# Optimization experiments

Hardware: AMD Instinct MI355X
Metric: run time of the kernel (lower is better)

Reference implementation:

```python
import jax, jax.numpy as jnp
import numpy as np

D_MODEL = 1024
SEL_DIM = 64
CONFIGS = [(4, 32), (8, 64), (16, 128)]  # (heads, dim)
B, T = 2, 2048


def setup_inputs() -> dict:
    key = jax.random.key(0)
    ks = jax.random.split(key, 20)
    s = 0.02  # init scale for stability
    inp = {
        "x": jax.random.normal(ks[0], (B, T, D_MODEL), jnp.float32),
        "sel_w1": jax.random.normal(ks[1], (SEL_DIM, D_MODEL), jnp.float32) * s,
        "sel_b1": jnp.zeros((SEL_DIM,), jnp.float32),
        "sel_w2": jax.random.normal(ks[2], (SEL_DIM, SEL_DIM), jnp.float32) * s,
        "sel_b2": jnp.zeros((SEL_DIM,), jnp.float32),
        "sel_w3": jax.random.normal(ks[3], (len(CONFIGS), SEL_DIM), jnp.float32) * s,
        "sel_b3": jnp.zeros((len(CONFIGS),), jnp.float32),
    }
    for i, (h, d) in enumerate(CONFIGS):
        inp[f"qw{i}"] = jax.random.normal(ks[4 + 3 * i], (h * d, D_MODEL), jnp.float32) * s
        inp[f"kw{i}"] = jax.random.normal(ks[5 + 3 * i], (d, D_MODEL), jnp.float32) * s
        inp[f"ww{i}"] = jax.random.normal(ks[6 + 3 * i], (h, D_MODEL), jnp.float32) * s
    return inp


def _seq_features(x):
    # x: [b,t,d]
    b, t, d = x.shape
    seq_mean = jnp.mean(x, axis=1, keepdims=True)            # [b,1,d]
    seq_std = jnp.std(x, axis=1, keepdims=True, ddof=1)      # torch.std is unbiased
    pos = (jnp.arange(t, dtype=x.dtype) / t)[None, :, None]  # [1,t,1] broadcast to [b,t,d]
    return x + seq_mean + seq_std + pos * 0.1


def _forward(x, sel_w1, sel_b1, sel_w2, sel_b2, sel_w3, sel_b3,
             qw0, kw0, ww0, qw1, kw1, ww1, qw2, kw2, ww2):
    b, t, dm = x.shape
    feats = _seq_features(x)
    h1 = jax.nn.relu(feats @ sel_w1.T + sel_b1)
    h2 = jax.nn.relu(h1 @ sel_w2.T + sel_b2)
    config_probs = jax.nn.softmax(h2 @ sel_w3.T + sel_b3, axis=-1)  # [b,t,ncfg]

    per_cfg = [(qw0, kw0, ww0), (qw1, kw1, ww1), (qw2, kw2, ww2)]
    final = jnp.zeros((b, t, t), dtype=x.dtype)
    for i, ((heads, dim), (qw, kw, ww)) in enumerate(zip(CONFIGS, per_cfg)):
        q = (x @ qw.T).reshape(b, t, heads, dim)   # [b,t,h,d]
        k = x @ kw.T                               # [b,s,d]
        w = x @ ww.T                               # [b,t,h]
        dots = jnp.einsum('bthd,bsd->bths', q, k)  # [b,t,h,s]
        score = jnp.einsum('bths,bth->bts', jax.nn.relu(dots), w)  # relu*weight, sum heads
        final = final + config_probs[:, :, i:i + 1] * score
    return final


def reference(x, sel_w1, sel_b1, sel_w2, sel_b2, sel_w3, sel_b3,
              qw0, kw0, ww0, qw1, kw1, ww1, qw2, kw2, ww2):
    return _forward(x, sel_w1, sel_b1, sel_w2, sel_b2, sel_w3, sel_b3,
                    qw0, kw0, ww0, qw1, kw1, ww1, qw2, kw2, ww2)
```

## Files before the change

### kernel.cpp

```cpp
#include <hip/hip_runtime.h>
#include <hip/hip_fp16.h>
#include <cstdint>
#include <cstddef>
#include <math.h>

#define B_ 2
#define T_ 2048
#define D_ 1024
#define M_ (B_*T_)

#define QO0 0
#define KO0 128
#define WO0 160
#define QO1 168
#define KO1 680
#define WO1 744
#define QO2 752
#define KO2 2800
#define WO2 2928
#define SELO 2944
#define LDN 3072

typedef float f32x16 __attribute__((ext_vector_type(16)));
typedef short bf16x8 __attribute__((ext_vector_type(8)));
typedef unsigned short u16;

__device__ __forceinline__ u16 f2bf(float f) {
    unsigned int u = __float_as_uint(f);
    unsigned int r = (u + 0x7fffu + ((u >> 16) & 1u)) >> 16;
    return (u16)r;
}
__device__ __forceinline__ float bf2f(u16 b) {
    return __uint_as_float(((unsigned int)b) << 16);
}

__device__ __forceinline__ void gload16(const void* g, void* l) {
    __builtin_amdgcn_global_load_lds(
        (const __attribute__((address_space(1))) unsigned int*)g,
        (__attribute__((address_space(3))) unsigned int*)l,
        16, 0, 0);
}

__device__ __forceinline__ void stage_plane(const u16* src_base, int row_stride, int k0,
                                            int rg, int lane, u16* dst) {
    int rl  = lane >> 2;
    int row = rg * 16 + rl;
    int q   = (lane & 3) ^ (rl & 3) ^ ((rl >> 2) & 3);
    const u16* s = src_base + (size_t)row * row_stride + k0 + q * 8;
    gload16(s, dst + rg * 512);
}

__global__ void stats1(const float* __restrict__ x, float* __restrict__ part,
                       float* __restrict__ part2, u16* __restrict__ Xh) {
    int d4 = threadIdx.x * 4;
    int tc = blockIdx.x;
    int b  = blockIdx.y;
    size_t base = (size_t)b * T_ * D_ + (size_t)tc * 16 * D_ + d4;
    float4 s = make_float4(0.f, 0.f, 0.f, 0.f);
    float4 s2 = make_float4(0.f, 0.f, 0.f, 0.f);
#pragma unroll
    for (int t = 0; t < 16; ++t) {
        float4 v = *(const float4*)(x + base + (size_t)t * D_);
        s.x += v.x; s.y += v.y; s.z += v.z; s.w += v.w;
        s2.x += v.x * v.x; s2.y += v.y * v.y; s2.z += v.z * v.z; s2.w += v.w * v.w;
        ushort4 h;
        h.x = f2bf(v.x); h.y = f2bf(v.y); h.z = f2bf(v.z); h.w = f2bf(v.w);
        *(ushort4*)(Xh + base + (size_t)t * D_) = h;
    }
    *(float4*)(part  + (size_t)(b * 128 + tc) * D_ + d4) = s;
    *(float4*)(part2 + (size_t)(b * 128 + tc) * D_ + d4) = s2;
}

__global__ void stats2(const float* __restrict__ part, const float* __restrict__ part2,
                       const float* __restrict__ w1,
                       float* __restrict__ msd, float* __restrict__ s1) {
    __shared__ float msL[1024];
    __shared__ float ps[64][17];
    __shared__ float pw[64][17];
    int b = blockIdx.x, tid = threadIdx.x;
    float s = 0.f, s2 = 0.f;
#pragma unroll 8
    for (int i = 0; i < 128; ++i) {
        s  += part [(b * 128 + i) * D_ + tid];
        s2 += part2[(b * 128 + i) * D_ + tid];
    }
    float mean = s / (float)T_;
    float var  = (s2 - (float)T_ * mean * mean) / (float)(T_ - 1);
    msL[tid] = mean + sqrtf(fmaxf(var, 0.f));
    __syncthreads();
    int j = tid >> 4, cc = tid & 15;
    float am = 0.f, aw = 0.f;
    const float* wr = w1 + (size_t)j * D_ + cc * 64;
    const float* mr = msL + cc * 64;
    for (int dd = 0; dd < 64; ++dd) { float w = wr[dd]; am += mr[dd] * w; aw += w; }
    ps[j][cc] = am; pw[j][cc] = aw;
    __syncthreads();
    if (tid < 64) {
        float sm = 0.f, sw = 0.f;
        for (int i = 0; i < 16; ++i) { sm += ps[tid][i]; sw += pw[tid][i]; }
        msd[b * 64 + tid] = sm;
        if (b == 0) s1[tid] = sw;
    }
}

__global__ void split_w(const float* __restrict__ qw0, const float* __restrict__ kw0,
                        const float* __restrict__ ww0, const float* __restrict__ qw1,
                        const float* __restrict__ kw1, const float* __restrict__ ww1,
                        const float* __restrict__ qw2, const float* __restrict__ kw2,
                        const float* __restrict__ ww2, const float* __restrict__ w1s,
                        u16* __restrict__ Wh) {
    int row = blockIdx.x;
    int col = threadIdx.x * 4;
    const float* src = nullptr;
    if      (row < 128)  src = qw0 + (size_t)row * D_;
    else if (row < 160)  src = kw0 + (size_t)(row - 128) * D_;
    else if (row < 164)  src = ww0 + (size_t)(row - 160) * D_;
    else if (row < 168)  src = nullptr;
    else if (row < 680)  src = qw1 + (size_t)(row - 168) * D_;
    else if (row < 744)  src = kw1 + (size_t)(row - 680) * D_;
    else if (row < 752)  src = ww1 + (size_t)(row - 744) * D_;
    else if (row < 2800) src = qw2 + (size_t)(row - 752) * D_;
    else if (row < 2928) src = kw2 + (size_t)(row - 2800) * D_;
    else if (row < 2944) src = ww2 + (size_t)(row - 2928) * D_;
    else if (row < 3008) src = w1s + (size_t)(row - 2944) * D_;
    float4 v = src ? *(const float4*)(src + col) : make_float4(0.f, 0.f, 0.f, 0.f);
    ushort4 h;
    h.x = f2bf(v.x); h.y = f2bf(v.y); h.z = f2bf(v.z); h.w = f2bf(v.w);
    *(ushort4*)&Wh[(size_t)row * D_ + col] = h;
}

__global__ __launch_bounds__(256, 3) void proj_gemm(
    const u16* __restrict__ Xh, const u16* __restrict__ Wh, u16* __restrict__ Ph) {
    __shared__ u16 As[8192], Bs[8192];
    int tid = threadIdx.x;
    int wave = tid >> 6, lane = tid & 63;
    int bm = blockIdx.x * 128, bn = blockIdx.y * 128;
    int wt = wave >> 1, wn = wave & 1;
    int fm = lane & 31, hv = lane >> 5;
    int tkey = (fm & 3) ^ ((fm >> 2) & 3);
    f32x16 acc[2][2];
#pragma unroll
    for (int i = 0; i < 2; ++i)
#pragma unroll
        for (int j = 0; j < 2; ++j)
#pragma unroll
            for (int r = 0; r < 16; ++r) acc[i][j][r] = 0.f;

    const u16* xh = Xh + (size_t)bm * D_;
    const u16* wh = Wh + (size_t)bn * D_;

    for (int kc = 0; kc < 16; ++kc) {
        int k0 = kc * 64;
#pragma unroll
        for (int i = 0; i < 8; ++i) {
            int j = wave * 8 + i;
            int mat = j >> 4;
            int pl  = (j >> 3) & 1;
            int rg  = j & 7;
            stage_plane(mat ? wh : xh, D_, k0 + pl * 32, rg, lane,
                        (mat ? Bs : As) + pl * 4096);
        }
        __syncthreads();
#pragma unroll
        for (int ks = 0; ks < 4; ++ks) {
            int pl = ks >> 1;
            int slot8 = (((ks & 1) * 2 + hv) ^ tkey) * 8;
            bf16x8 a_h[2], b_h[2];
#pragma unroll
            for (int t = 0; t < 2; ++t) {
                a_h[t] = *(const bf16x8*)&As[pl * 4096 + (wt * 64 + t * 32 + fm) * 32 + slot8];
                b_h[t] = *(const bf16x8*)&Bs[pl * 4096 + (wn * 64 + t * 32 + fm) * 32 + slot8];
            }
#pragma unroll
            for (int ti = 0; ti < 2; ++ti)
#pragma unroll
                for (int tj = 0; tj < 2; ++tj)
                    acc[ti][tj] = __builtin_amdgcn_mfma_f32_32x32x16_bf16(a_h[ti], b_h[tj], acc[ti][tj], 0, 0, 0);
        }
        __syncthreads();
    }
#pragma unroll
    for (int ti = 0; ti < 2; ++ti)
#pragma unroll
        for (int tj = 0; tj < 2; ++tj)
#pragma unroll
            for (int r = 0; r < 16; ++r) {
                int row = bm + wt * 64 + ti * 32 + (r & 3) + 8 * (r >> 2) + 4 * hv;
                int col = bn + wn * 64 + tj * 32 + fm;
                Ph[(size_t)row * LDN + col] = f2bf(acc[ti][tj][r]);
            }
}

__global__ void selector2(const u16* __restrict__ Ph,
                          const float* __restrict__ msd, const float* __restrict__ s1,
                          const float* __restrict__ b1, const float* __restrict__ w2,
                          const float* __restrict__ b2, const float* __restrict__ w3,
                          const float* __restrict__ b3, __half* __restrict__ WP) {
    __shared__ float h1s[4][64];
    __shared__ float h2s[4][64];
    __shared__ float lg[4][3];
    int tid = threadIdx.x;
    int slot = tid >> 6, j = tid & 63;
    int bt = blockIdx.x * 4 + slot;
    int b = bt >> 11, t = bt & 2047;
    size_t pidx = (size_t)bt * LDN + SELO + j;
    float v = bf2f(Ph[pidx])
            + msd[b * 64 + j] + 0.1f * ((float)t / (float)T_) * s1[j] + b1[j];
    h1s[slot][j] = fmaxf(v, 0.f);
    __syncthreads();
    float a2 = b2[j];
    {
        const float4* w2v = (const float4*)(w2 + (size_t)j * 64);
        const float4* h1v = (const float4*)h1s[slot];
#pragma unroll
        for (int d = 0; d < 16; ++d) {
            float4 wv = w2v[d], hv4 = h1v[d];
            a2 = fmaf(hv4.x, wv.x, a2);
            a2 = fmaf(hv4.y, wv.y, a2);
            a2 = fmaf(hv4.z, wv.z, a2);
            a2 = fmaf(hv4.w, wv.w, a2);
        }
    }
    h2s[slot][j] = fmaxf(a2, 0.f);
    __syncthreads();
    if (j < 3) {
        float a3 = b3[j];
        const float4* w3v = (const float4*)(w3 + (size_t)j * 64);
        const float4* h2v = (const float4*)h2s[slot];
#pragma unroll
        for (int d = 0; d < 16; ++d) {
            float4 wv = w3v[d], hv4 = h2v[d];
            a3 = fmaf(hv4.x, wv.x, a3);
            a3 = fmaf(hv4.y, wv.y, a3);
            a3 = fmaf(hv4.z, wv.z, a3);
            a3 = fmaf(hv4.w, wv.w, a3);
        }
        lg[slot][j] = a3;
    }
    __syncthreads();
    if (j < 28) {
        float m = fmaxf(lg[slot][0], fmaxf(lg[slot][1], lg[slot][2]));
        float e0 = expf(lg[slot][0] - m), e1 = expf(lg[slot][1] - m), e2 = expf(lg[slot][2] - m);
        float inv = 1.f / (e0 + e1 + e2);
        int wcol = (j < 4) ? (WO0 + j) : ((j < 12) ? (WO1 + j - 4) : (WO2 + j - 12));
        float p = ((j < 4) ? e0 : ((j < 12) ? e1 : e2)) * inv;
        float w = bf2f(Ph[(size_t)bt * LDN + wcol]);
        WP[(size_t)(b * 28 + j) * T_ + t] = __float2half(w * p);
    }
}

__device__ __forceinline__ int qcol_of(int c) {
    if (c < 2)  return QO0 + c * 64;
    if (c < 10) return QO1 + (c - 2) * 64;
    return QO2 + (c - 10) * 64;
}

__global__ __launch_bounds__(256, 2) void score_kernel(
    const u16* __restrict__ Ph, const __half* __restrict__ WP, float* __restrict__ out) {
    __shared__ u16 Qs[2][8192];
    __shared__ u16 Ks[4 * 4096];
    __shared__ __half wpL[3584];
    int tid = threadIdx.x;
    int wave = tid >> 6, lane = tid & 63;
    int wt = wave >> 1, wn = wave & 1;
    int fm = lane & 31, hv = lane >> 5;
    int tkey = (fm & 3) ^ ((fm >> 2) & 3);

    int n = blockIdx.z * 256 + blockIdx.y * 16 + blockIdx.x;
    int p = (n & 7) * 4 + (n >> 7);
    int xb = (n >> 3) & 15;
    int b = p >> 4, yb = p & 15;
    int t0 = yb * 128, s0 = xb * 128;

    const u16* Pq = Ph + (size_t)(b * T_ + t0) * LDN;
    const u16* Pk = Ph + (size_t)(b * T_ + s0) * LDN;

    auto stageQ = [&](int buf, int qcol) {
#pragma unroll
        for (int i = 0; i < 4; ++i) {
            int j = (wave << 2) + i;
            int pl = j >> 3, rg = j & 7;
            stage_plane(Pq, LDN, qcol + pl * 32, rg, lane, &Qs[buf][pl * 4096]);
        }
    };

#pragma unroll
    for (int i = 0; i < 6; ++i) {
        int j = i * 4 + wave;
        int pl = j >> 3, rg = j & 7;
        int col = (pl == 0) ? KO0 : ((pl == 1) ? KO1 : KO1 + 32);
        stage_plane(Pk, LDN, col, rg, lane, &Ks[pl * 4096]);
    }
#pragma unroll
    for (int i = 0; i < 2; ++i) {
        int j = i * 4 + wave;
        if (j < 7) {
            const __half* src = WP + (size_t)(b * 28 + j * 4 + (lane >> 4)) * T_ + t0 + (lane & 15) * 8;
            gload16(src, (u16*)wpL + j * 512);
        }
    }
    stageQ(0, QO0);

    f32x16 outacc[2][2], dots[2][2], Z16;
#pragma unroll
    for (int r = 0; r < 16; ++r) Z16[r] = 0.f;
#pragma unroll
    for (int i = 0; i < 2; ++i)
#pragma unroll
        for (int j = 0; j < 2; ++j)
#pragma unroll
            for (int r = 0; r < 16; ++r) { outacc[i][j][r] = 0.f; dots[i][j][r] = 0.f; }

    auto epi = [&](int g) {
#pragma unroll
        for (int ti = 0; ti < 2; ++ti) {
            int rowbase = wt * 64 + ti * 32 + 4 * hv;
#pragma unroll
            for (int rq = 0; rq < 4; ++rq) {
                __half2 wpq[2];
                *(short4*)wpq = *(const short4*)&wpL[g * 128 + rowbase + rq * 8];
                float2 f01 = __half22float2(wpq[0]);
                float2 f23 = __half22float2(wpq[1]);
                float wv[4] = {f01.x, f01.y, f23.x, f23.y};
#pragma unroll
                for (int tj = 0; tj < 2; ++tj)
#pragma unroll
                    for (int r2 = 0; r2 < 4; ++r2) {
                        int r = rq * 4 + r2;
                        outacc[ti][tj][r] += fmaxf(dots[ti][tj][r], 0.f) * wv[r2];
                    }
            }
        }
    };

    auto runPhase = [&](int c, int kpA, int kpB, bool z0, bool midBreak,
                        int gMid, bool hasEnd, int gEnd) {
        if (c + 1 < 42) {
            stageQ((c + 1) & 1, qcol_of(c + 1));
            asm volatile("s_waitcnt vmcnt(4)" ::: "memory");
        } else {
            asm volatile("s_waitcnt vmcnt(0)" ::: "memory");
        }
        __builtin_amdgcn_s_barrier();
        __builtin_amdgcn_sched_barrier(0);
        const u16* qb = Qs[c & 1];

        bf16x8 kf[2][2], qf[2][2];
        auto loadks = [&](int ks, int sl) {
            int kp = (ks < 2) ? kpA : kpB;
            int slot8 = (((ks & 1) * 2 + hv) ^ tkey) * 8;
#pragma unroll
            for (int tj = 0; tj < 2; ++tj)
                kf[sl][tj] = *(const bf16x8*)&Ks[kp * 4096 + (wn * 64 + tj * 32 + fm) * 32 + slot8];
#pragma unroll
            for (int ti = 0; ti < 2; ++ti)
                qf[sl][ti] = *(const bf16x8*)&qb[(ks >> 1) * 4096 + (wt * 64 + ti * 32 + fm) * 32 + slot8];
        };
        loadks(0, 0);
#pragma unroll
        for (int ks = 0; ks < 4; ++ks) {
            if (ks < 3) loadks(ks + 1, (ks + 1) & 1);
            bool zero = (ks == 0 && z0) || (ks == 2 && midBreak);
            int sl = ks & 1;
            __builtin_amdgcn_s_setprio(1);
#pragma unroll
            for (int ti = 0; ti < 2; ++ti)
#pragma unroll
                for (int tj = 0; tj < 2; ++tj)
                    dots[ti][tj] = __builtin_amdgcn_mfma_f32_32x32x16_bf16(
                        qf[sl][ti], kf[sl][tj], zero ? Z16 : dots[ti][tj], 0, 0, 0);
            __builtin_amdgcn_s_setprio(0);
            if (ks == 1 && midBreak) epi(gMid);
            if (ks == 3 && hasEnd)   epi(gEnd);
        }
        __builtin_amdgcn_sched_barrier(0);
        __builtin_amdgcn_s_barrier();
    };

#pragma unroll
    for (int c = 0; c < 2; ++c)
        runPhase(c, 0, 0, true, true, 2 * c, true, 2 * c + 1);
    for (int h = 0; h < 8; ++h) {
        runPhase(2 + h, 1, 2, true, false, -1, true, 4 + h);
        if (h == 7) {
            for (int j = wave; j < 32; j += 4) {
                int pl = j >> 3, rg = j & 7;
                stage_plane(Pk, LDN, KO2 + pl * 32, rg, lane, &Ks[pl * 4096]);
            }
        }
    }
    for (int h = 0; h < 16; ++h) {
        runPhase(10 + 2 * h, 0, 1, true, false, -1, false, -1);
        runPhase(11 + 2 * h, 2, 3, false, false, -1, true, 12 + h);
    }

#pragma unroll
    for (int ti = 0; ti < 2; ++ti)
#pragma unroll
        for (int tj = 0; tj < 2; ++tj)
#pragma unroll
            for (int r = 0; r < 16; ++r) {
                int trow = wt * 64 + ti * 32 + (r & 3) + 8 * (r >> 2) + 4 * hv;
                int scol = wn * 64 + tj * 32 + fm;
                __builtin_nontemporal_store(outacc[ti][tj][r],
                    &out[(size_t)(b * T_ + t0 + trow) * T_ + (s0 + scol)]);
            }
}

extern "C" void kernel_launch(void* const* d_in, const int* in_sizes, int n_in,
                              void* d_out, int out_size, void* d_ws, size_t ws_size,
                              hipStream_t stream) {
    const float* x   = (const float*)d_in[0];
    const float* w1  = (const float*)d_in[1];
    const float* b1  = (const float*)d_in[2];
    const float* w2  = (const float*)d_in[3];
    const float* b2  = (const float*)d_in[4];
    const float* w3  = (const float*)d_in[5];
    const float* b3  = (const float*)d_in[6];
    const float* qw0 = (const float*)d_in[7];
    const float* kw0 = (const float*)d_in[8];
    const float* ww0 = (const float*)d_in[9];
    const float* qw1 = (const float*)d_in[10];
    const float* kw1 = (const float*)d_in[11];
    const float* ww1 = (const float*)d_in[12];
    const float* qw2 = (const float*)d_in[13];
    const float* kw2 = (const float*)d_in[14];
    const float* ww2 = (const float*)d_in[15];
    float* out = (float*)d_out;

    float* fb = (float*)d_ws;
    float* PA  = fb; fb += (size_t)B_ * 128 * D_;
    float* PA2 = fb; fb += (size_t)B_ * 128 * D_;
    float* MSD = fb; fb += 128;
    float* S1  = fb; fb += 64;
    __half* WP = (__half*)fb; fb += (size_t)B_ * 28 * T_ / 2;
    u16* ub = (u16*)fb;
    u16* Wh = ub; ub += (size_t)LDN * D_;
    u16* Xh = ub; ub += (size_t)M_ * D_;
    u16* Ph = ub; ub += (size_t)M_ * LDN;

    stats1<<<dim3(128, B_), 256, 0, stream>>>(x, PA, PA2, Xh);
    stats2<<<dim3(B_), 1024, 0, stream>>>(PA, PA2, w1, MSD, S1);
    split_w<<<dim3(LDN), 256, 0, stream>>>(qw0, kw0, ww0, qw1, kw1, ww1,
                                           qw2, kw2, ww2, w1, Wh);
    proj_gemm<<<dim3(M_ / 128, LDN / 128), 256, 0, stream>>>(Xh, Wh, Ph);
    selector2<<<dim3(M_ / 4), 256, 0, stream>>>(Ph, MSD, S1, b1, w2, b2, w3, b3, WP);
    score_kernel<<<dim3(T_ / 128, T_ / 128, B_), 256, 0, stream>>>(Ph, WP, out);
}
```

Before: 256.4 us.

## Fuse stats and weight-cast kernels; precompute LDS pointers and fp32 weights in score kernel

Merges stats1 and split_w into a single prep launch, which removes one kernel launch and lets the two independent jobs run concurrently. In score_kernel, the per-head weight tile is converted to fp32 in LDS once up front instead of being converted in the epilogue. Per-lane global and LDS base pointers are now precomputed, so the inner loop does less address arithmetic. The fragment double-buffering (prefetching the next k-step's loads) is dropped in favour of straight loads per k-step. This adds a __syncthreads and doubles the wp LDS footprint, and it risks exposing more LDS latency because the loads are no longer prefetched.

```diff
diff --git a/kernel.cpp b/kernel.cpp
--- a/kernel.cpp
+++ b/kernel.cpp
@@ -50,25 +50,53 @@
     gload16(s, dst + rg * 512);
 }
 
-__global__ void stats1(const float* __restrict__ x, float* __restrict__ part,
-                       float* __restrict__ part2, u16* __restrict__ Xh) {
-    int d4 = threadIdx.x * 4;
-    int tc = blockIdx.x;
-    int b  = blockIdx.y;
-    size_t base = (size_t)b * T_ * D_ + (size_t)tc * 16 * D_ + d4;
-    float4 s = make_float4(0.f, 0.f, 0.f, 0.f);
-    float4 s2 = make_float4(0.f, 0.f, 0.f, 0.f);
-#pragma unroll
-    for (int t = 0; t < 16; ++t) {
-        float4 v = *(const float4*)(x + base + (size_t)t * D_);
-        s.x += v.x; s.y += v.y; s.z += v.z; s.w += v.w;
-        s2.x += v.x * v.x; s2.y += v.y * v.y; s2.z += v.z * v.z; s2.w += v.w * v.w;
+__global__ void prep(const float* __restrict__ x, float* __restrict__ part,
+                     float* __restrict__ part2, u16* __restrict__ Xh,
+                     const float* __restrict__ qw0, const float* __restrict__ kw0,
+                     const float* __restrict__ ww0, const float* __restrict__ qw1,
+                     const float* __restrict__ kw1, const float* __restrict__ ww1,
+                     const float* __restrict__ qw2, const float* __restrict__ kw2,
+                     const float* __restrict__ ww2, const float* __restrict__ w1s,
+                     u16* __restrict__ Wh) {
+    int bid = blockIdx.x;
+    if (bid < 256) {
+        int d4 = threadIdx.x * 4;
+        int tc = bid & 127;
+        int b  = bid >> 7;
+        size_t base = (size_t)b * T_ * D_ + (size_t)tc * 16 * D_ + d4;
+        float4 s = make_float4(0.f, 0.f, 0.f, 0.f);
+        float4 s2 = make_float4(0.f, 0.f, 0.f, 0.f);
+#pragma unroll
+        for (int t = 0; t < 16; ++t) {
+            float4 v = *(const float4*)(x + base + (size_t)t * D_);
+            s.x += v.x; s.y += v.y; s.z += v.z; s.w += v.w;
+            s2.x += v.x * v.x; s2.y += v.y * v.y; s2.z += v.z * v.z; s2.w += v.w * v.w;
+            ushort4 h;
+            h.x = f2bf(v.x); h.y = f2bf(v.y); h.z = f2bf(v.z); h.w = f2bf(v.w);
+            *(ushort4*)(Xh + base + (size_t)t * D_) = h;
+        }
+        *(float4*)(part  + (size_t)(b * 128 + tc) * D_ + d4) = s;
+        *(float4*)(part2 + (size_t)(b * 128 + tc) * D_ + d4) = s2;
+    } else {
+        int row = bid - 256;
+        int col = threadIdx.x * 4;
+        const float* src = nullptr;
+        if      (row < 128)  src = qw0 + (size_t)row * D_;
+        else if (row < 160)  src = kw0 + (size_t)(row - 128) * D_;
+        else if (row < 164)  src = ww0 + (size_t)(row - 160) * D_;
+        else if (row < 168)  src = nullptr;
+        else if (row < 680)  src = qw1 + (size_t)(row - 168) * D_;
+        else if (row < 744)  src = kw1 + (size_t)(row - 680) * D_;
+        else if (row < 752)  src = ww1 + (size_t)(row - 744) * D_;
+        else if (row < 2800) src = qw2 + (size_t)(row - 752) * D_;
+        else if (row < 2928) src = kw2 + (size_t)(row - 2800) * D_;
+        else if (row < 2944) src = ww2 + (size_t)(row - 2928) * D_;
+        else if (row < 3008) src = w1s + (size_t)(row - 2944) * D_;
+        float4 v = src ? *(const float4*)(src + col) : make_float4(0.f, 0.f, 0.f, 0.f);
         ushort4 h;
         h.x = f2bf(v.x); h.y = f2bf(v.y); h.z = f2bf(v.z); h.w = f2bf(v.w);
-        *(ushort4*)(Xh + base + (size_t)t * D_) = h;
-    }
-    *(float4*)(part  + (size_t)(b * 128 + tc) * D_ + d4) = s;
-    *(float4*)(part2 + (size_t)(b * 128 + tc) * D_ + d4) = s2;
+        *(ushort4*)&Wh[(size_t)row * D_ + col] = h;
+    }
 }
 
 __global__ void stats2(const float* __restrict__ part, const float* __restrict__ part2,
@@ -101,32 +129,6 @@
         msd[b * 64 + tid] = sm;
         if (b == 0) s1[tid] = sw;
     }
-}
-
-__global__ void split_w(const float* __restrict__ qw0, const float* __restrict__ kw0,
-                        const float* __restrict__ ww0, const float* __restrict__ qw1,
-                        const float* __restrict__ kw1, const float* __restrict__ ww1,
-                        const float* __restrict__ qw2, const float* __restrict__ kw2,
-                        const float* __restrict__ ww2, const float* __restrict__ w1s,
-                        u16* __restrict__ Wh) {
-    int row = blockIdx.x;
-    int col = threadIdx.x * 4;
-    const float* src = nullptr;
-    if      (row < 128)  src = qw0 + (size_t)row * D_;
-    else if (row < 160)  src = kw0 + (size_t)(row - 128) * D_;
-    else if (row < 164)  src = ww0 + (size_t)(row - 160) * D_;
-    else if (row < 168)  src = nullptr;
-    else if (row < 680)  src = qw1 + (size_t)(row - 168) * D_;
-    else if (row < 744)  src = kw1 + (size_t)(row - 680) * D_;
-    else if (row < 752)  src = ww1 + (size_t)(row - 744) * D_;
-    else if (row < 2800) src = qw2 + (size_t)(row - 752) * D_;
-    else if (row < 2928) src = kw2 + (size_t)(row - 2800) * D_;
-    else if (row < 2944) src = ww2 + (size_t)(row - 2928) * D_;
-    else if (row < 3008) src = w1s + (size_t)(row - 2944) * D_;
-    float4 v = src ? *(const float4*)(src + col) : make_float4(0.f, 0.f, 0.f, 0.f);
-    ushort4 h;
-    h.x = f2bf(v.x); h.y = f2bf(v.y); h.z = f2bf(v.z); h.w = f2bf(v.w);
-    *(ushort4*)&Wh[(size_t)row * D_ + col] = h;
 }
 
 __global__ __launch_bounds__(256, 3) void proj_gemm(
@@ -259,7 +261,7 @@
     const u16* __restrict__ Ph, const __half* __restrict__ WP, float* __restrict__ out) {
     __shared__ u16 Qs[2][8192];
     __shared__ u16 Ks[4 * 4096];
-    __shared__ __half wpL[3584];
+    __shared__ __align__(16) float wpF[3584];
     int tid = threadIdx.x;
     int wave = tid >> 6, lane = tid & 63;
     int wt = wave >> 1, wn = wave & 1;
@@ -275,31 +277,55 @@
     const u16* Pq = Ph + (size_t)(b * T_ + t0) * LDN;
     const u16* Pk = Ph + (size_t)(b * T_ + s0) * LDN;
 
+    int rl = lane >> 2;
+    int q8 = ((lane & 3) ^ (rl & 3) ^ ((rl >> 2) & 3)) * 8;
+    const u16* PqL = Pq + (size_t)rl * LDN + q8;
+    const u16* PkL = Pk + (size_t)rl * LDN + q8;
+
     auto stageQ = [&](int buf, int qcol) {
 #pragma unroll
         for (int i = 0; i < 4; ++i) {
             int j = (wave << 2) + i;
             int pl = j >> 3, rg = j & 7;
-            stage_plane(Pq, LDN, qcol + pl * 32, rg, lane, &Qs[buf][pl * 4096]);
+            gload16(PqL + (size_t)(rg * 16) * LDN + pl * 32 + qcol,
+                    &Qs[buf][pl * 4096 + rg * 512]);
         }
     };
 
+#pragma unroll
+    for (int r = 0; r < 14; ++r) {
+        int e = r * 256 + tid;
+        int jj = e >> 7, ii = e & 127;
+        wpF[e] = __half2float(WP[(size_t)(b * 28 + jj) * T_ + t0 + ii]);
+    }
 #pragma unroll
     for (int i = 0; i < 6; ++i) {
         int j = i * 4 + wave;
         int pl = j >> 3, rg = j & 7;
         int col = (pl == 0) ? KO0 : ((pl == 1) ? KO1 : KO1 + 32);
-        stage_plane(Pk, LDN, col, rg, lane, &Ks[pl * 4096]);
-    }
-#pragma unroll
-    for (int i = 0; i < 2; ++i) {
-        int j = i * 4 + wave;
-        if (j < 7) {
-            const __half* src = WP + (size_t)(b * 28 + j * 4 + (lane >> 4)) * T_ + t0 + (lane & 15) * 8;
-            gload16(src, (u16*)wpL + j * 512);
-        }
+        gload16(PkL + (size_t)(rg * 16) * LDN + col, &Ks[pl * 4096 + rg * 512]);
     }
     stageQ(0, QO0);
+    __syncthreads();
+
+    int slotE = (hv ^ tkey) * 8;
+    int slotO = ((2 + hv) ^ tkey) * 8;
+    const u16 *kB_E[2], *kB_O[2], *qB_E[2][2], *qB_O[2][2];
+#pragma unroll
+    for (int tj = 0; tj < 2; ++tj) {
+        int row = (wn * 64 + tj * 32 + fm) * 32;
+        kB_E[tj] = Ks + row + slotE;
+        kB_O[tj] = Ks + row + slotO;
+    }
+#pragma unroll
+    for (int ti = 0; ti < 2; ++ti) {
+        int row = (wt * 64 + ti * 32 + fm) * 32;
+#pragma unroll
+        for (int bf = 0; bf < 2; ++bf) {
+            qB_E[bf][ti] = &Qs[bf][row + slotE];
+            qB_O[bf][ti] = &Qs[bf][row + slotO];
+        }
+    }
 
     f32x16 outacc[2][2], dots[2][2], Z16;
 #pragma unroll
@@ -317,11 +343,8 @@
             int rowbase = wt * 64 + ti * 32 + 4 * hv;
 #pragma unroll
             for (int rq = 0; rq < 4; ++rq) {
-                __half2 wpq[2];
-                *(short4*)wpq = *(const short4*)&wpL[g * 128 + rowbase + rq * 8];
-                float2 f01 = __half22float2(wpq[0]);
-                float2 f23 = __half22float2(wpq[1]);
-                float wv[4] = {f01.x, f01.y, f23.x, f23.y};
+                float4 wv4 = *(const float4*)&wpF[g * 128 + rowbase + rq * 8];
+                float wv[4] = {wv4.x, wv4.y, wv4.z, wv4.w};
 #pragma unroll
                 for (int tj = 0; tj < 2; ++tj)
 #pragma unroll
@@ -333,7 +356,8 @@
         }
     };
 
-    auto runPhase = [&](int c, int kpA, int kpB, bool z0, bool midBreak,
+    auto runPhase = [&](int c, const u16* const* qE, const u16* const* qO,
+                        int kpA, int kpB, bool z0, bool midBreak,
                         int gMid, bool hasEnd, int gEnd) {
         if (c + 1 < 42) {
             stageQ((c + 1) & 1, qcol_of(c + 1));
@@ -343,32 +367,26 @@
         }
         __builtin_amdgcn_s_barrier();
         __builtin_amdgcn_sched_barrier(0);
-        const u16* qb = Qs[c & 1];
-
-        bf16x8 kf[2][2], qf[2][2];
-        auto loadks = [&](int ks, int sl) {
+
+#pragma unroll
+        for (int ks = 0; ks < 4; ++ks) {
             int kp = (ks < 2) ? kpA : kpB;
-            int slot8 = (((ks & 1) * 2 + hv) ^ tkey) * 8;
+            bool odd = ks & 1;
+            bf16x8 kf[2], qf[2];
 #pragma unroll
             for (int tj = 0; tj < 2; ++tj)
-                kf[sl][tj] = *(const bf16x8*)&Ks[kp * 4096 + (wn * 64 + tj * 32 + fm) * 32 + slot8];
+                kf[tj] = *(const bf16x8*)((odd ? kB_O[tj] : kB_E[tj]) + kp * 4096);
 #pragma unroll
             for (int ti = 0; ti < 2; ++ti)
-                qf[sl][ti] = *(const bf16x8*)&qb[(ks >> 1) * 4096 + (wt * 64 + ti * 32 + fm) * 32 + slot8];
-        };
-        loadks(0, 0);
-#pragma unroll
-        for (int ks = 0; ks < 4; ++ks) {
-            if (ks < 3) loadks(ks + 1, (ks + 1) & 1);
+                qf[ti] = *(const bf16x8*)((odd ? qO[ti] : qE[ti]) + (ks >> 1) * 4096);
             bool zero = (ks == 0 && z0) || (ks == 2 && midBreak);
-            int sl = ks & 1;
             __builtin_amdgcn_s_setprio(1);
 #pragma unroll
             for (int ti = 0; ti < 2; ++ti)
 #pragma unroll
                 for (int tj = 0; tj < 2; ++tj)
                     dots[ti][tj] = __builtin_amdgcn_mfma_f32_32x32x16_bf16(
-                        qf[sl][ti], kf[sl][tj], zero ? Z16 : dots[ti][tj], 0, 0, 0);
+                        qf[ti], kf[tj], zero ? Z16 : dots[ti][tj], 0, 0, 0);
             __builtin_amdgcn_s_setprio(0);
             if (ks == 1 && midBreak) epi(gMid);
             if (ks == 3 && hasEnd)   epi(gEnd);
@@ -377,21 +395,22 @@
         __builtin_amdgcn_s_barrier();
     };
 
-#pragma unroll
-    for (int c = 0; c < 2; ++c)
-        runPhase(c, 0, 0, true, true, 2 * c, true, 2 * c + 1);
-    for (int h = 0; h < 8; ++h) {
-        runPhase(2 + h, 1, 2, true, false, -1, true, 4 + h);
-        if (h == 7) {
+    runPhase(0, qB_E[0], qB_O[0], 0, 0, true, true, 0, true, 1);
+    runPhase(1, qB_E[1], qB_O[1], 0, 0, true, true, 2, true, 3);
+    for (int h = 0; h < 8; h += 2) {
+        runPhase(2 + h, qB_E[0], qB_O[0], 1, 2, true, false, -1, true, 4 + h);
+        runPhase(3 + h, qB_E[1], qB_O[1], 1, 2, true, false, -1, true, 5 + h);
+        if (h == 6) {
             for (int j = wave; j < 32; j += 4) {
                 int pl = j >> 3, rg = j & 7;
-                stage_plane(Pk, LDN, KO2 + pl * 32, rg, lane, &Ks[pl * 4096]);
+                gload16(PkL + (size_t)(rg * 16) * LDN + KO2 + pl * 32,
+                        &Ks[pl * 4096 + rg * 512]);
             }
         }
     }
     for (int h = 0; h < 16; ++h) {
-        runPhase(10 + 2 * h, 0, 1, true, false, -1, false, -1);
-        runPhase(11 + 2 * h, 2, 3, false, false, -1, true, 12 + h);
+        runPhase(10 + 2 * h, qB_E[0], qB_O[0], 0, 1, true, false, -1, false, -1);
+        runPhase(11 + 2 * h, qB_E[1], qB_O[1], 2, 3, false, false, -1, true, 12 + h);
     }
 
 #pragma unroll
@@ -439,10 +458,10 @@
     u16* Xh = ub; ub += (size_t)M_ * D_;
     u16* Ph = ub; ub += (size_t)M_ * LDN;
 
-    stats1<<<dim3(128, B_), 256, 0, stream>>>(x, PA, PA2, Xh);
+    prep<<<dim3(256 + LDN), 256, 0, stream>>>(x, PA, PA2, Xh,
+                                              qw0, kw0, ww0, qw1, kw1, ww1,
+                                              qw2, kw2, ww2, w1, Wh);
     stats2<<<dim3(B_), 1024, 0, stream>>>(PA, PA2, w1, MSD, S1);
-    split_w<<<dim3(LDN), 256, 0, stream>>>(qw0, kw0, ww0, qw1, kw1, ww1,
-                                           qw2, kw2, ww2, w1, Wh);
     proj_gemm<<<dim3(M_ / 128, LDN / 128), 256, 0, stream>>>(Xh, Wh, Ph);
     selector2<<<dim3(M_ / 4), 256, 0, stream>>>(Ph, MSD, S1, b1, w2, b2, w3, b3, WP);
     score_kernel<<<dim3(T_ / 128, T_ / 128, B_), 256, 0, stream>>>(Ph, WP, out);
```

After: 268.0 us. +4.5%, slower.
